# Performance work log

Hardware: AMD Instinct MI355X
Metric: run time of the kernel (lower is better)

Reference implementation:

```python
import jax, jax.numpy as jnp
import numpy as np

D_MODEL = 1024
N_HEADS = 16
DEPTH = D_MODEL // N_HEADS
NEG_INF = -1.0e9


def setup_inputs() -> dict:
    key = jax.random.key(0)
    ks = jax.random.split(key, 11)
    B, S = 2, 2048
    xk = jax.random.normal(ks[0], (B, S, D_MODEL), jnp.float32)
    xq = jax.random.normal(ks[1], (B, S, D_MODEL), jnp.float32)
    xv = jax.random.normal(ks[2], (B, S, D_MODEL), jnp.float32)
    sc = 1.0 / np.sqrt(D_MODEL)
    wq = jax.random.normal(ks[3], (D_MODEL, D_MODEL), jnp.float32) * sc
    wk = jax.random.normal(ks[4], (D_MODEL, D_MODEL), jnp.float32) * sc
    wv = jax.random.normal(ks[5], (D_MODEL, D_MODEL), jnp.float32) * sc
    wo = jax.random.normal(ks[6], (D_MODEL, D_MODEL), jnp.float32) * sc
    bq = jnp.zeros((D_MODEL,), jnp.float32)
    bk = jnp.zeros((D_MODEL,), jnp.float32)
    bv = jnp.zeros((D_MODEL,), jnp.float32)
    bo = jnp.zeros((D_MODEL,), jnp.float32)
    return {"xk": xk, "xq": xq, "xv": xv, "wq": wq, "bq": bq, "wk": wk,
            "bk": bk, "wv": wv, "bv": bv, "wo": wo, "bo": bo}


def _split_heads(t):
    # [B, S, D] -> [B, H, S, depth]
    B, S, _ = t.shape
    return t.reshape(B, S, N_HEADS, DEPTH).transpose(0, 2, 1, 3)


def reference(xk, xq, xv, wq, bq, wk, bk, wv, bv, wo, bo):
    B, Sq, _ = xq.shape
    Sk = xk.shape[1]
    q = _split_heads(xq @ wq + bq)  # [B,H,Sq,d]
    k = _split_heads(xk @ wk + bk)  # [B,H,Sk,d]
    v = _split_heads(xv @ wv + bv)  # [B,H,Sk,d]
    logits = jnp.einsum('bhqd,bhkd->bhqk', q, k) / jnp.sqrt(
        jnp.asarray(DEPTH, q.dtype))
    # additive causal mask: (1 - lower_triangular) * -1e9
    causal = (1.0 - jnp.tril(jnp.ones((Sq, Sk), logits.dtype))) * NEG_INF
    logits = logits + causal[None, None, :, :]
    attn = jax.nn.softmax(logits, axis=-1)
    out = jnp.einsum('bhqk,bhkd->bhqd', attn, v)
    out = out.transpose(0, 2, 1, 3).reshape(B, Sq, D_MODEL)
    return out @ wo + bo
```

## Files before the change

### kernel.cpp

```cpp
#include <hip/hip_runtime.h>

typedef unsigned short u16;
typedef u16 u16x8 __attribute__((ext_vector_type(8)));
typedef __bf16 bf16x8 __attribute__((ext_vector_type(8)));
typedef float f32x4 __attribute__((ext_vector_type(4)));

#define DM 1024
#define SEQ 2048
#define BATCH 2
#define MROWS 4096

__device__ __forceinline__ u16 f2bf(float f) {
  unsigned int x = __builtin_bit_cast(unsigned int, f);
  x += 0x7fffu + ((x >> 16) & 1u);
  return (u16)(x >> 16);
}
__device__ __forceinline__ u16 f2bf_trunc(float f) {
  return (u16)(__builtin_bit_cast(unsigned int, f) >> 16);
}

__device__ __forceinline__ void gld16(const void* g, void* l) {
  __builtin_amdgcn_global_load_lds(
      (const __attribute__((address_space(1))) void*)g,
      (__attribute__((address_space(3))) void*)l, 16, 0, 0);
}

struct TrArgs { const float* in[4]; u16* out[4]; };

__global__ __launch_bounds__(256) void transpose_w4(TrArgs a) {
  const float* __restrict__ in = a.in[blockIdx.z];
  u16* __restrict__ out = a.out[blockIdx.z];
  __shared__ u16 T[64][72];
  int r0 = blockIdx.y * 64, c0 = blockIdx.x * 64;
  int t = threadIdx.x;
  int r = t >> 3, cg = (t & 7) * 8;
#pragma unroll
  for (int p = 0; p < 2; p++) {
    const float* src = in + (size_t)(r0 + r + p * 32) * DM + c0 + cg;
    f32x4 x0 = *(const f32x4*)src;
    f32x4 x1 = *(const f32x4*)(src + 4);
    u16x8 v;
#pragma unroll
    for (int j = 0; j < 4; j++) { v[j] = f2bf(x0[j]); v[4 + j] = f2bf(x1[j]); }
    *(u16x8*)(&T[r + p * 32][cg]) = v;
  }
  __syncthreads();
#pragma unroll
  for (int p = 0; p < 2; p++) {
    int orow = r + p * 32;
    u16x8 v;
#pragma unroll
    for (int j = 0; j < 8; j++) v[j] = T[cg + j][orow];
    *(u16x8*)(out + (size_t)(c0 + orow) * DM + r0 + cg) = v;
  }
}

struct CastArgs { const float* in[3]; u16* out[3]; };

__global__ __launch_bounds__(256) void cast_x(CastArgs a) {
  const float* __restrict__ in = a.in[blockIdx.y];
  u16* __restrict__ out = a.out[blockIdx.y];
  size_t e = ((size_t)blockIdx.x * 256 + threadIdx.x) * 8;
  f32x4 a0 = *(const f32x4*)(in + e);
  f32x4 a1 = *(const f32x4*)(in + e + 4);
  u16x8 v;
#pragma unroll
  for (int j = 0; j < 4; j++) { v[j] = f2bf(a0[j]); v[4 + j] = f2bf(a1[j]); }
  *(u16x8*)(out + e) = v;
}

struct GemmArgs { const void* A[3]; const u16* WT[3]; const float* bias[3]; void* C[3]; };

template <int MT, int NT, bool AF32, bool OF32>
__global__ __launch_bounds__(256) void gemmT(GemmArgs g) {
  __shared__ __align__(16) u16 As[MT * 32 * 32];
  __shared__ __align__(16) u16 Bs[NT * 32 * 32];
  const int z = blockIdx.z;
  const u16* __restrict__ WT = g.WT[z];
  const int tid = threadIdx.x;
  const int lane = tid & 63, wave = tid >> 6;
  const int fr = lane & 15, kq = lane >> 4;
  const int mq = (wave >> 1) * (MT * 16), nq = (wave & 1) * (NT * 16);
  const int m0 = blockIdx.y * (MT * 32), n0 = blockIdx.x * (NT * 32);
  const int srow = tid >> 2;
  const int scA = ((tid & 3) ^ ((srow >> 1) & 3)) * 8;
  const int fco = ((kq ^ ((fr >> 1) & 3)) * 8);
  f32x4 acc[MT][NT] = {};

  for (int kk = 0; kk < DM; kk += 32) {
    __syncthreads();
    if constexpr (AF32) {
      const float* A = (const float*)g.A[z];
#pragma unroll
      for (int i = 0; i < MT / 2; i++) {
        const float* s0 = A + (size_t)(m0 + i * 64 + srow) * DM + kk + scA;
        f32x4 a0 = *(const f32x4*)s0, a1 = *(const f32x4*)(s0 + 4);
        u16x8 v;
#pragma unroll
        for (int j = 0; j < 4; j++) { v[j] = f2bf(a0[j]); v[4 + j] = f2bf(a1[j]); }
        *(u16x8*)(As + (i * 256 + tid) * 8) = v;
      }
    } else {
      const u16* A = (const u16*)g.A[z];
#pragma unroll
      for (int i = 0; i < MT / 2; i++)
        gld16(A + (size_t)(m0 + i * 64 + srow) * DM + kk + scA,
              As + (i * 256 + tid) * 8);
    }
#pragma unroll
    for (int i = 0; i < NT / 2; i++)
      gld16(WT + (size_t)(n0 + i * 64 + srow) * DM + kk + scA,
            Bs + (i * 256 + tid) * 8);
    __syncthreads();
    bf16x8 af[MT], bfr[NT];
#pragma unroll
    for (int mt = 0; mt < MT; mt++)
      af[mt] = __builtin_bit_cast(
          bf16x8, *(const u16x8*)(As + (mq + mt * 16 + fr) * 32 + fco));
#pragma unroll
    for (int nt = 0; nt < NT; nt++)
      bfr[nt] = __builtin_bit_cast(
          bf16x8, *(const u16x8*)(Bs + (nq + nt * 16 + fr) * 32 + fco));
#pragma unroll
    for (int mt = 0; mt < MT; mt++)
#pragma unroll
      for (int nt = 0; nt < NT; nt++)
        acc[mt][nt] =
            __builtin_amdgcn_mfma_f32_16x16x32_bf16(af[mt], bfr[nt], acc[mt][nt], 0, 0, 0);
  }
  const float* __restrict__ bias = g.bias[z];
#pragma unroll
  for (int nt = 0; nt < NT; nt++) {
    int col = n0 + nq + nt * 16 + fr;
    float bb = bias[col];
#pragma unroll
    for (int mt = 0; mt < MT; mt++)
#pragma unroll
      for (int r = 0; r < 4; r++) {
        int row = m0 + mq + mt * 16 + kq * 4 + r;
        float val = acc[mt][nt][r] + bb;
        if constexpr (OF32)
          ((float*)g.C[z])[(size_t)row * DM + col] = val;
        else
          ((u16*)g.C[z])[(size_t)row * DM + col] = f2bf(val);
      }
  }
}

#define KS 72
__global__ __launch_bounds__(256) void attn3(u16* __restrict__ Q,
                                             const u16* __restrict__ K,
                                             const u16* __restrict__ V) {
  __shared__ __align__(16) u16 Ksh[2][64 * 64];
  __shared__ __align__(16) u16 Vt[2][64 * KS];
  __shared__ __align__(16) u16 Ps[4][16 * KS];
  const int tid = threadIdx.x, wave = tid >> 6, lane = tid & 63;
  const int fr = lane & 15, kq = lane >> 4;
  const int b = blockIdx.x >> 4, h = blockIdx.x & 15;
  const int qt = 31 - blockIdx.y;
  const float C1 = 0.125f * 1.44269504f;

  const int krow = tid >> 3;
  const int kcs = ((tid & 7) ^ (krow & 7)) * 8;
  const u16* Kg = K + (size_t)(b * SEQ + krow) * DM + h * 64 + kcs;
  const u16* Vg = V + (size_t)(b * SEQ + lane) * DM + h * 64 + wave * 16;

  const int f7 = fr & 7;
  const int x0 = (kq ^ f7) * 8;
  const int x1 = ((4 + kq) ^ f7) * 8;

  bf16x8 qf0, qf1;
  {
    size_t qr = (size_t)(b * SEQ + qt * 64 + wave * 16 + fr) * DM + h * 64;
    qf0 = __builtin_bit_cast(bf16x8, *(const u16x8*)(Q + qr + kq * 8));
    qf1 = __builtin_bit_cast(bf16x8, *(const u16x8*)(Q + qr + 32 + kq * 8));
  }

  u16x8 onesu;
#pragma unroll
  for (int j = 0; j < 8; j++) onesu[j] = 0x3F80;
  const bf16x8 vones = __builtin_bit_cast(bf16x8, onesu);

  f32x4 ov[5] = {};
  u16* Pw = Ps[wave];

  gld16(Kg, Ksh[0] + tid * 8);
  gld16(Kg + (size_t)32 * DM, Ksh[0] + (256 + tid) * 8);
  {
    u16x8 v0 = *(const u16x8*)(Vg);
    u16x8 v1 = *(const u16x8*)(Vg + 8);
#pragma unroll
    for (int j = 0; j < 8; j++) {
      Vt[0][(wave * 16 + j) * KS + lane] = v0[j];
      Vt[0][(wave * 16 + 8 + j) * KS + lane] = v1[j];
    }
  }
  __syncthreads();

  int cur = 0;
  for (int t = 0; t <= qt; t++) {
    const int nb = cur ^ 1;
    u16x8 nv0, nv1;
    const bool pf = (t < qt);
    if (pf) {
      size_t ro = (size_t)(t + 1) * 64 * DM;
      gld16(Kg + ro, Ksh[nb] + tid * 8);
      gld16(Kg + ro + (size_t)32 * DM, Ksh[nb] + (256 + tid) * 8);
      nv0 = *(const u16x8*)(Vg + ro);
      nv1 = *(const u16x8*)(Vg + ro + 8);
    }
    const u16* Kc = Ksh[cur];
    f32x4 sv[4];
#pragma unroll
    for (int nt = 0; nt < 4; nt++) {
      f32x4 s = {};
      bf16x8 b0 = __builtin_bit_cast(
          bf16x8, *(const u16x8*)(Kc + (nt * 16 + fr) * 64 + x0));
      s = __builtin_amdgcn_mfma_f32_16x16x32_bf16(qf0, b0, s, 0, 0, 0);
      bf16x8 b1 = __builtin_bit_cast(
          bf16x8, *(const u16x8*)(Kc + (nt * 16 + fr) * 64 + x1));
      s = __builtin_amdgcn_mfma_f32_16x16x32_bf16(qf1, b1, s, 0, 0, 0);
      sv[nt] = s;
    }
    if (t == qt) {
#pragma unroll
      for (int nt = 0; nt < 4; nt++)
#pragma unroll
        for (int r = 0; r < 4; r++)
          if (nt * 16 + fr > wave * 16 + kq * 4 + r) sv[nt][r] = -1e30f;
    }
#pragma unroll
    for (int nt = 0; nt < 4; nt++)
#pragma unroll
      for (int r = 0; r < 4; r++) {
        float pp = __builtin_amdgcn_exp2f(sv[nt][r] * C1);
        Pw[(kq * 4 + r) * KS + nt * 16 + fr] = f2bf_trunc(pp);
      }
    const u16* Vc = Vt[cur];
#pragma unroll
    for (int kk = 0; kk < 2; kk++) {
      bf16x8 pa = __builtin_bit_cast(
          bf16x8, *(const u16x8*)(Pw + fr * KS + kk * 32 + kq * 8));
#pragma unroll
      for (int nt = 0; nt < 4; nt++) {
        bf16x8 vb = __builtin_bit_cast(
            bf16x8, *(const u16x8*)(Vc + (nt * 16 + fr) * KS + kk * 32 + kq * 8));
        ov[nt] = __builtin_amdgcn_mfma_f32_16x16x32_bf16(pa, vb, ov[nt], 0, 0, 0);
      }
      ov[4] = __builtin_amdgcn_mfma_f32_16x16x32_bf16(pa, vones, ov[4], 0, 0, 0);
    }
    if (pf) {
#pragma unroll
      for (int j = 0; j < 8; j++) {
        Vt[nb][(wave * 16 + j) * KS + lane] = nv0[j];
        Vt[nb][(wave * 16 + 8 + j) * KS + lane] = nv1[j];
      }
    }
    __syncthreads();
    cur = nb;
  }
  float rinv[4];
#pragma unroll
  for (int r = 0; r < 4; r++) rinv[r] = 1.0f / ov[4][r];
#pragma unroll
  for (int nt = 0; nt < 4; nt++)
#pragma unroll
    for (int r = 0; r < 4; r++) {
      int row = qt * 64 + wave * 16 + kq * 4 + r;
      Q[(size_t)(b * SEQ + row) * DM + h * 64 + nt * 16 + fr] =
          f2bf(ov[nt][r] * rinv[r]);
    }
}

extern "C" void kernel_launch(void* const* d_in, const int* in_sizes, int n_in,
                              void* d_out, int out_size, void* d_ws,
                              size_t ws_size, hipStream_t stream) {
  const float* xk = (const float*)d_in[0];
  const float* xq = (const float*)d_in[1];
  const float* xv = (const float*)d_in[2];
  const float* wq = (const float*)d_in[3];
  const float* bq = (const float*)d_in[4];
  const float* wk = (const float*)d_in[5];
  const float* bk = (const float*)d_in[6];
  const float* wv = (const float*)d_in[7];
  const float* bv = (const float*)d_in[8];
  const float* wo = (const float*)d_in[9];
  const float* bo = (const float*)d_in[10];

  u16* Qb = (u16*)d_ws;
  u16* Kb = Qb + (size_t)MROWS * DM;
  u16* Vb = Kb + (size_t)MROWS * DM;
  u16* WTq = Vb + (size_t)MROWS * DM;
  u16* WTk = WTq + (size_t)DM * DM;
  u16* WTv = WTk + (size_t)DM * DM;
  u16* WTo = WTv + (size_t)DM * DM;
  u16* Xq = WTo + (size_t)DM * DM;
  u16* Xk = Xq + (size_t)MROWS * DM;
  u16* Xv = Xk + (size_t)MROWS * DM;
  const bool cast_path =
      ws_size >= ((size_t)(3 * 8 + 4 * 2 + 3 * 8)) * 1024 * 1024;

  dim3 blk(256);

  TrArgs tr;
  tr.in[0] = wq; tr.in[1] = wk; tr.in[2] = wv; tr.in[3] = wo;
  tr.out[0] = WTq; tr.out[1] = WTk; tr.out[2] = WTv; tr.out[3] = WTo;
  transpose_w4<<<dim3(16, 16, 4), blk, 0, stream>>>(tr);

  GemmArgs gq;
  gq.WT[0] = WTq; gq.WT[1] = WTk; gq.WT[2] = WTv;
  gq.bias[0] = bq; gq.bias[1] = bk; gq.bias[2] = bv;
  gq.C[0] = Qb; gq.C[1] = Kb; gq.C[2] = Vb;
  if (cast_path) {
    CastArgs ca;
    ca.in[0] = xq; ca.in[1] = xk; ca.in[2] = xv;
    ca.out[0] = Xq; ca.out[1] = Xk; ca.out[2] = Xv;
    cast_x<<<dim3(MROWS * DM / 2048, 3), blk, 0, stream>>>(ca);
    gq.A[0] = Xq; gq.A[1] = Xk; gq.A[2] = Xv;
    gemmT<4, 4, false, false>
        <<<dim3(DM / 128, MROWS / 128, 3), blk, 0, stream>>>(gq);
  } else {
    gq.A[0] = xq; gq.A[1] = xk; gq.A[2] = xv;
    gemmT<4, 4, true, false>
        <<<dim3(DM / 128, MROWS / 128, 3), blk, 0, stream>>>(gq);
  }

  attn3<<<dim3(BATCH * 16, 32), blk, 0, stream>>>(Qb, Kb, Vb);

  GemmArgs go;
  go.A[0] = Qb;  go.WT[0] = WTo; go.bias[0] = bo; go.C[0] = d_out;
  go.A[1] = Qb;  go.WT[1] = WTo; go.bias[1] = bo; go.C[1] = d_out;
  go.A[2] = Qb;  go.WT[2] = WTo; go.bias[2] = bo; go.C[2] = d_out;
  gemmT<2, 4, false, true>
      <<<dim3(DM / 128, MROWS / 64, 1), blk, 0, stream>>>(go);
}
```

Baseline: 219.2 us.

## Switch attention to 32x32 MFMA with register-resident P via permlane swap

The attention kernel now uses 32x32x16 bf16 MFMAs and computes S transposed (K as A operand), so each block handles 128 query rows instead of 64. The probability tile no longer goes through LDS: it is packed with v_cvt_pk_bf16_f32 and rearranged with v_permlane32_swap so it can feed the PV MFMA directly from registers. Each K/V tile loaded into LDS is therefore reused by twice as many queries and the per-wave P store/load round-trip is gone. The cost is half as many blocks (512), with coarser causal load imbalance and higher register pressure from the 16-wide accumulators.

```diff
diff --git a/kernel.cpp b/kernel.cpp
--- a/kernel.cpp
+++ b/kernel.cpp
@@ -1,9 +1,12 @@
 #include <hip/hip_runtime.h>
 
 typedef unsigned short u16;
+typedef unsigned int u32;
 typedef u16 u16x8 __attribute__((ext_vector_type(8)));
+typedef u32 u32x4 __attribute__((ext_vector_type(4)));
 typedef __bf16 bf16x8 __attribute__((ext_vector_type(8)));
 typedef float f32x4 __attribute__((ext_vector_type(4)));
+typedef float f32x16 __attribute__((ext_vector_type(16)));
 
 #define DM 1024
 #define SEQ 2048
@@ -15,14 +18,20 @@
   x += 0x7fffu + ((x >> 16) & 1u);
   return (u16)(x >> 16);
 }
-__device__ __forceinline__ u16 f2bf_trunc(float f) {
-  return (u16)(__builtin_bit_cast(unsigned int, f) >> 16);
-}
 
 __device__ __forceinline__ void gld16(const void* g, void* l) {
   __builtin_amdgcn_global_load_lds(
       (const __attribute__((address_space(1))) void*)g,
       (__attribute__((address_space(3))) void*)l, 16, 0, 0);
+}
+
+__device__ __forceinline__ u32 cvtpk_bf16(float lo, float hi) {
+  u32 r;
+  asm("v_cvt_pk_bf16_f32 %0, %1, %2" : "=v"(r) : "v"(lo), "v"(hi));
+  return r;
+}
+__device__ __forceinline__ void pl32swap(u32& x, u32& y) {
+  asm volatile("v_permlane32_swap_b32 %0, %1" : "+v"(x), "+v"(y));
 }
 
 struct TrArgs { const float* in[4]; u16* out[4]; };
@@ -153,11 +162,11 @@
                                              const u16* __restrict__ V) {
   __shared__ __align__(16) u16 Ksh[2][64 * 64];
   __shared__ __align__(16) u16 Vt[2][64 * KS];
-  __shared__ __align__(16) u16 Ps[4][16 * KS];
   const int tid = threadIdx.x, wave = tid >> 6, lane = tid & 63;
-  const int fr = lane & 15, kq = lane >> 4;
+  const int ql = lane & 31, hi = lane >> 5;
   const int b = blockIdx.x >> 4, h = blockIdx.x & 15;
-  const int qt = 31 - blockIdx.y;
+  const int qt = 15 - blockIdx.y;
+  const int tmax = 2 * qt + 1;
   const float C1 = 0.125f * 1.44269504f;
 
   const int krow = tid >> 3;
@@ -165,15 +174,17 @@
   const u16* Kg = K + (size_t)(b * SEQ + krow) * DM + h * 64 + kcs;
   const u16* Vg = V + (size_t)(b * SEQ + lane) * DM + h * 64 + wave * 16;
 
-  const int f7 = fr & 7;
-  const int x0 = (kq ^ f7) * 8;
-  const int x1 = ((4 + kq) ^ f7) * 8;
-
-  bf16x8 qf0, qf1;
+  int xsl[4];
+#pragma unroll
+  for (int f = 0; f < 4; f++) xsl[f] = ((2 * f + hi) ^ (ql & 7)) * 8;
+
+  bf16x8 qf[4];
   {
-    size_t qr = (size_t)(b * SEQ + qt * 64 + wave * 16 + fr) * DM + h * 64;
-    qf0 = __builtin_bit_cast(bf16x8, *(const u16x8*)(Q + qr + kq * 8));
-    qf1 = __builtin_bit_cast(bf16x8, *(const u16x8*)(Q + qr + 32 + kq * 8));
+    size_t qr = (size_t)(b * SEQ + qt * 128 + wave * 32 + ql) * DM + h * 64;
+#pragma unroll
+    for (int f = 0; f < 4; f++)
+      qf[f] = __builtin_bit_cast(bf16x8,
+                                 *(const u16x8*)(Q + qr + f * 16 + hi * 8));
   }
 
   u16x8 onesu;
@@ -181,8 +192,7 @@
   for (int j = 0; j < 8; j++) onesu[j] = 0x3F80;
   const bf16x8 vones = __builtin_bit_cast(bf16x8, onesu);
 
-  f32x4 ov[5] = {};
-  u16* Pw = Ps[wave];
+  f32x16 ov0 = {}, ov1 = {}, ovl = {};
 
   gld16(Kg, Ksh[0] + tid * 8);
   gld16(Kg + (size_t)32 * DM, Ksh[0] + (256 + tid) * 8);
@@ -198,10 +208,10 @@
   __syncthreads();
 
   int cur = 0;
-  for (int t = 0; t <= qt; t++) {
+  for (int t = 0; t <= tmax; t++) {
     const int nb = cur ^ 1;
     u16x8 nv0, nv1;
-    const bool pf = (t < qt);
+    const bool pf = (t < tmax);
     if (pf) {
       size_t ro = (size_t)(t + 1) * 64 * DM;
       gld16(Kg + ro, Ksh[nb] + tid * 8);
@@ -210,45 +220,54 @@
       nv1 = *(const u16x8*)(Vg + ro + 8);
     }
     const u16* Kc = Ksh[cur];
-    f32x4 sv[4];
-#pragma unroll
-    for (int nt = 0; nt < 4; nt++) {
-      f32x4 s = {};
-      bf16x8 b0 = __builtin_bit_cast(
-          bf16x8, *(const u16x8*)(Kc + (nt * 16 + fr) * 64 + x0));
-      s = __builtin_amdgcn_mfma_f32_16x16x32_bf16(qf0, b0, s, 0, 0, 0);
-      bf16x8 b1 = __builtin_bit_cast(
-          bf16x8, *(const u16x8*)(Kc + (nt * 16 + fr) * 64 + x1));
-      s = __builtin_amdgcn_mfma_f32_16x16x32_bf16(qf1, b1, s, 0, 0, 0);
-      sv[nt] = s;
-    }
-    if (t == qt) {
-#pragma unroll
-      for (int nt = 0; nt < 4; nt++)
-#pragma unroll
-        for (int r = 0; r < 4; r++)
-          if (nt * 16 + fr > wave * 16 + kq * 4 + r) sv[nt][r] = -1e30f;
-    }
-#pragma unroll
-    for (int nt = 0; nt < 4; nt++)
-#pragma unroll
-      for (int r = 0; r < 4; r++) {
-        float pp = __builtin_amdgcn_exp2f(sv[nt][r] * C1);
-        Pw[(kq * 4 + r) * KS + nt * 16 + fr] = f2bf_trunc(pp);
+    f32x16 s0 = {}, s1 = {};
+#pragma unroll
+    for (int f = 0; f < 4; f++) {
+      bf16x8 a0 = __builtin_bit_cast(
+          bf16x8, *(const u16x8*)(Kc + ql * 64 + xsl[f]));
+      s0 = __builtin_amdgcn_mfma_f32_32x32x16_bf16(a0, qf[f], s0, 0, 0, 0);
+      bf16x8 a1 = __builtin_bit_cast(
+          bf16x8, *(const u16x8*)(Kc + (32 + ql) * 64 + xsl[f]));
+      s1 = __builtin_amdgcn_mfma_f32_32x32x16_bf16(a1, qf[f], s1, 0, 0, 0);
+    }
+    if (t >= 2 * qt) {
+      int qg = qt * 128 + wave * 32 + ql;
+      int kb = t * 64 + 4 * hi;
+#pragma unroll
+      for (int r = 0; r < 16; r++) {
+        int key = kb + (r & 3) + 8 * (r >> 2);
+        if (key > qg) s0[r] = -1e30f;
+        if (key + 32 > qg) s1[r] = -1e30f;
       }
+    }
     const u16* Vc = Vt[cur];
-#pragma unroll
-    for (int kk = 0; kk < 2; kk++) {
-      bf16x8 pa = __builtin_bit_cast(
-          bf16x8, *(const u16x8*)(Pw + fr * KS + kk * 32 + kq * 8));
-#pragma unroll
-      for (int nt = 0; nt < 4; nt++) {
-        bf16x8 vb = __builtin_bit_cast(
-            bf16x8, *(const u16x8*)(Vc + (nt * 16 + fr) * KS + kk * 32 + kq * 8));
-        ov[nt] = __builtin_amdgcn_mfma_f32_16x16x32_bf16(pa, vb, ov[nt], 0, 0, 0);
-      }
-      ov[4] = __builtin_amdgcn_mfma_f32_16x16x32_bf16(pa, vones, ov[4], 0, 0, 0);
-    }
+#define DO_NT(SV, KB)                                                        \
+  {                                                                          \
+    float p[16];                                                             \
+    _Pragma("unroll") for (int r = 0; r < 16; r++)                           \
+        p[r] = __builtin_amdgcn_exp2f(SV[r] * C1);                           \
+    _Pragma("unroll") for (int s = 0; s < 2; s++) {                          \
+      u32 w0 = cvtpk_bf16(p[s * 8 + 0], p[s * 8 + 1]);                       \
+      u32 w1 = cvtpk_bf16(p[s * 8 + 2], p[s * 8 + 3]);                       \
+      u32 w2 = cvtpk_bf16(p[s * 8 + 4], p[s * 8 + 5]);                       \
+      u32 w3 = cvtpk_bf16(p[s * 8 + 6], p[s * 8 + 7]);                       \
+      pl32swap(w0, w2);                                                      \
+      pl32swap(w1, w3);                                                      \
+      u32x4 paw = {w0, w1, w2, w3};                                          \
+      bf16x8 pa = __builtin_bit_cast(bf16x8, paw);                           \
+      const int kb2 = (KB) + s * 16 + hi * 8;                                \
+      bf16x8 vb0 = __builtin_bit_cast(                                       \
+          bf16x8, *(const u16x8*)(Vc + ql * KS + kb2));                      \
+      ov0 = __builtin_amdgcn_mfma_f32_32x32x16_bf16(pa, vb0, ov0, 0, 0, 0);  \
+      bf16x8 vb1 = __builtin_bit_cast(                                       \
+          bf16x8, *(const u16x8*)(Vc + (32 + ql) * KS + kb2));               \
+      ov1 = __builtin_amdgcn_mfma_f32_32x32x16_bf16(pa, vb1, ov1, 0, 0, 0);  \
+      ovl = __builtin_amdgcn_mfma_f32_32x32x16_bf16(pa, vones, ovl, 0, 0, 0); \
+    }                                                                        \
+  }
+    DO_NT(s0, 0)
+    DO_NT(s1, 32)
+#undef DO_NT
     if (pf) {
 #pragma unroll
       for (int j = 0; j < 8; j++) {
@@ -259,17 +278,16 @@
     __syncthreads();
     cur = nb;
   }
-  float rinv[4];
-#pragma unroll
-  for (int r = 0; r < 4; r++) rinv[r] = 1.0f / ov[4][r];
-#pragma unroll
-  for (int nt = 0; nt < 4; nt++)
-#pragma unroll
-    for (int r = 0; r < 4; r++) {
-      int row = qt * 64 + wave * 16 + kq * 4 + r;
-      Q[(size_t)(b * SEQ + row) * DM + h * 64 + nt * 16 + fr] =
-          f2bf(ov[nt][r] * rinv[r]);
-    }
+  float rinv[16];
+#pragma unroll
+  for (int r = 0; r < 16; r++) rinv[r] = 1.0f / ovl[r];
+#pragma unroll
+  for (int r = 0; r < 16; r++) {
+    int row = qt * 128 + wave * 32 + (r & 3) + 8 * (r >> 2) + 4 * hi;
+    size_t base = (size_t)(b * SEQ + row) * DM + h * 64 + ql;
+    Q[base] = f2bf(ov0[r] * rinv[r]);
+    Q[base + 32] = f2bf(ov1[r] * rinv[r]);
+  }
 }
 
 extern "C" void kernel_launch(void* const* d_in, const int* in_sizes, int n_in,
@@ -325,7 +343,7 @@
         <<<dim3(DM / 128, MROWS / 128, 3), blk, 0, stream>>>(gq);
   }
 
-  attn3<<<dim3(BATCH * 16, 32), blk, 0, stream>>>(Qb, Kb, Vb);
+  attn3<<<dim3(BATCH * 16, 16), blk, 0, stream>>>(Qb, Kb, Vb);
 
   GemmArgs go;
   go.A[0] = Qb;  go.WT[0] = WTo; go.bias[0] = bo; go.C[0] = d_out;
```

After: 228.6 us. 1.04x slower.
